# Kernel optimization log

Measured on AMD Instinct MI355X. Metric: run time of the kernel, lower is better.

## Reference

```python
import jax, jax.numpy as jnp
import numpy as np
from jax import lax

SIGMA1, SIGMA2, TRUNCATE = 4.2, 96.0, 4.0


def _gauss_kernel1d(sigma, truncate):
    # scipy-style: radius = int(truncate*sigma + 0.5), normalized Gaussian
    r = int(truncate * sigma + 0.5)
    t = jnp.arange(-r, r + 1, dtype=jnp.float32)
    k = jnp.exp(-0.5 * (t / sigma) ** 2)
    return k / jnp.sum(k)


def _depthwise_conv1d_centered(x_bcl, k):
    # x_bcl: [B, C, L]; k: [K] with K odd. Centered 'same' conv with reflect padding.
    B, C, L = x_bcl.shape
    K = k.shape[0]
    r = (K - 1) // 2
    xp = jnp.pad(x_bcl, ((0, 0), (0, 0), (r, r)), mode='reflect')
    w = jnp.broadcast_to(k[None, None, :], (C, 1, K)).astype(x_bcl.dtype)
    return lax.conv_general_dilated(
        xp, w, window_strides=(1,), padding='VALID',
        feature_group_count=C,
        dimension_numbers=('NCH', 'OIH', 'NCH'))


def setup_inputs() -> dict:
    key = jax.random.key(0)
    x = jax.random.normal(key, (32, 4096, 321), dtype=jnp.float32)  # [B, L, C]
    return {"x": x}


def reference(x) -> jnp.ndarray:
    k1 = _gauss_kernel1d(SIGMA1, TRUNCATE).astype(x.dtype)
    k2 = _gauss_kernel1d(SIGMA2, TRUNCATE).astype(x.dtype)
    x_bcl = jnp.transpose(x, (0, 2, 1))          # [B, C, L]
    y1 = _depthwise_conv1d_centered(x_bcl, k1)   # narrow Gaussian LP
    y2 = _depthwise_conv1d_centered(x_bcl, k2)   # wide Gaussian LP
    seasonal = y1 - y2
    return jnp.transpose(seasonal, (0, 2, 1))    # back to [B, L, C]
```

## Files before the change

### kernel.cpp

```cpp
#include <hip/hip_runtime.h>
#include <math.h>


#define Bdim 32
#define Ldim 4096
#define Cdim 321

#define R1 17
#define K1n 35
#define R2 384
#define K2n 769

#define GA_R 48
#define GA_N 97
#define GB_R 24
#define GB_N 49

#define NG 257
#define NJD 305
#define NGRP_A 20
#define NTJ 33

#define TL 64
#define TROWS 98
#define NLT 64
#define NCT 6
#define NSEG 128

#define GA_OFF 0
#define GB_OFF 128
#define W1_OFF 192
#define K2_OFF 256
#define K2P_OFF 1088
#define E2_OFF 4096
#define D_OFF 4096
#define E_OFF (D_OFF + Bdim*NJD*Cdim)
#define WS_TOT (E_OFF + Bdim*NG*Cdim)

typedef float f32x2 __attribute__((ext_vector_type(2)));

__device__ __forceinline__ int mirror_idx(int a) {
    a = a < 0 ? -a : a;
    a = a > (Ldim - 1) ? 2 * (Ldim - 1) - a : a;
    return a;
}

__device__ __forceinline__ int xcd_swizzle(int bid, int nwg) {
    int q = nwg >> 3, r = nwg & 7;
    int xcd = bid & 7, i = bid >> 3;
    int base = (xcd < r) ? xcd * (q + 1) : r * (q + 1) + (xcd - r) * q;
    return base + i;
}

__device__ __forceinline__ float block_sum_1024(float v, float* partial) {
#pragma unroll
    for (int off = 32; off >= 1; off >>= 1) v += __shfl_down(v, off, 64);
    __syncthreads();
    if ((threadIdx.x & 63) == 0) partial[threadIdx.x >> 6] = v;
    __syncthreads();
    float s = partial[0];
#pragma unroll
    for (int i = 1; i < 16; ++i) s += partial[i];
    return s;
}

__global__ void init_weights_kernel(float* __restrict__ w) {
    __shared__ float partial[16];
    const int tid = threadIdx.x;

    {
        float v = 0.f;
        if (tid < GA_N) { float t = (float)(tid - GA_R) * (1.0f / 12.0f); v = expf(-0.5f * t * t); }
        float s = block_sum_1024(v, partial);
        if (tid < GA_N) w[GA_OFF + tid] = v / s;
    }
    {
        const float sb = sqrtf(96.f * 96.f - 12.f * 12.f) * (1.0f / 16.0f);
        float v = 0.f;
        if (tid < GB_N) { float t = (float)(tid - GB_R) / sb; v = expf(-0.5f * t * t); }
        float s = block_sum_1024(v, partial);
        if (tid < GB_N) w[GB_OFF + tid] = v / s;
    }
    {
        float v = 0.f;
        if (tid < K1n) { float t = (float)(tid - R1) * (1.0f / 4.2f); v = expf(-0.5f * t * t); }
        float s = block_sum_1024(v, partial);
        if (tid < K1n) w[W1_OFF + tid] = v / s;
    }
    {
        float v = 0.f;
        if (tid < K2n) { float t = (float)(tid - R2) * (1.0f / 96.0f); v = expf(-0.5f * t * t); }
        float s = block_sum_1024(v, partial);
        if (tid < K2n) w[K2_OFF + tid] = v / s;
        if (tid < 784) w[K2P_OFF + tid] = (tid < K2n) ? v / s : 0.f;
    }
}

__global__ __launch_bounds__(256) void decimA_kernel(
        const float* __restrict__ x, const float* __restrict__ ga,
        float* __restrict__ d) {
    __shared__ float gs[GA_N];
    if (threadIdx.x < GA_N) gs[threadIdx.x] = ga[threadIdx.x];
    __syncthreads();

    const int lb = xcd_swizzle(blockIdx.x, gridDim.x);
    const int lin = lb * 256 + threadIdx.x;
    const int c = lin % Cdim;
    const int rest = lin / Cdim;
    const int g = rest % NGRP_A;
    const int b = rest / NGRP_A;
    if (b >= Bdim) return;

    const int jj0 = -24 + 16 * g;
    const float* xb = x + b * (Ldim * Cdim) + c;

    float acc[16];
#pragma unroll
    for (int ii = 0; ii < 16; ++ii) acc[ii] = 0.f;

    const bool interior = (jj0 >= 3) && (jj0 <= 237);

#pragma unroll 1
    for (int p = 0; p < 16; ++p) {
        float row[22];
        if (interior) {
            const float* xp = xb + (16 * (jj0 - 3) + p) * Cdim;
#pragma unroll
            for (int i = 0; i < 22; ++i) row[i] = xp[i * (16 * Cdim)];
        } else {
#pragma unroll
            for (int i = 0; i < 22; ++i)
                row[i] = xb[mirror_idx(16 * (jj0 - 3 + i) + p) * Cdim];
        }
#pragma unroll
        for (int q = 0; q < 6; ++q) {
            const float wq = gs[16 * q + p];
#pragma unroll
            for (int ii = 0; ii < 16; ++ii)
                acc[ii] = fmaf(wq, row[ii + q], acc[ii]);
        }
        if (p == 0) {
            const float w6 = gs[96];
#pragma unroll
            for (int ii = 0; ii < 16; ++ii)
                acc[ii] = fmaf(w6, row[ii + 6], acc[ii]);
        }
    }

    const int j0d = jj0 + 24;
    float* db = d + (b * NJD + j0d) * Cdim + c;
#pragma unroll
    for (int ii = 0; ii < 16; ++ii)
        if (j0d + ii < NJD) db[ii * Cdim] = acc[ii];
}

__global__ __launch_bounds__(256) void coarseB_kernel(
        const float* __restrict__ d, const float* __restrict__ gb,
        float* __restrict__ e) {
    __shared__ float gbs[GB_N];
    if (threadIdx.x < GB_N) gbs[threadIdx.x] = gb[threadIdx.x];
    __syncthreads();

    const int lin = blockIdx.x * 256 + threadIdx.x;
    const int c = lin % Cdim;
    const int rest = lin / Cdim;
    const int tj = rest % NTJ;
    const int b = rest / NTJ;
    if (b >= Bdim) return;

    const int j0 = tj * 8;
    const float* db = d + b * (NJD * Cdim) + c;

    float row[56];
#pragma unroll
    for (int r = 0; r < 56; ++r) {
        int idx = j0 + r;
        idx = idx > (NJD - 1) ? (NJD - 1) : idx;
        row[r] = db[idx * Cdim];
    }

    float acc[8];
#pragma unroll
    for (int jj = 0; jj < 8; ++jj) acc[jj] = 0.f;
#pragma unroll
    for (int s = 0; s < GB_N; ++s) {
        const float wv = gbs[s];
#pragma unroll
        for (int jj = 0; jj < 8; ++jj)
            acc[jj] = fmaf(wv, row[s + jj], acc[jj]);
    }

    float* eb = e + (b * NG + j0) * Cdim + c;
#pragma unroll
    for (int jj = 0; jj < 8; ++jj)
        if (j0 + jj < NG) eb[jj * Cdim] = acc[jj];
}

__global__ __launch_bounds__(256, 3) void narrow_lds_kernel(
        const float* __restrict__ x, const float* __restrict__ w1,
        const float* __restrict__ e, float* __restrict__ out) {
    __shared__ float ws[K1n];
    __shared__ float tile[TROWS * 64];
    if (threadIdx.x < K1n) ws[threadIdx.x] = w1[threadIdx.x];

    const int bid = xcd_swizzle(blockIdx.x, gridDim.x);
    const int lt = bid % NLT;
    const int rest = bid / NLT;
    const int ct = rest % NCT;
    const int b = rest / NCT;

    const int c = threadIdx.x & 63;
    const int wv = threadIdx.x >> 6;
    const int c0 = (ct < 5) ? ct * 64 : Cdim - 64;
    const int l0 = lt * TL;
    const float* xb = x + b * (Ldim * Cdim);

    if (lt > 0 && lt < NLT - 1) {
        const float* xp = xb + (l0 - R1) * Cdim + c0 + c;
#pragma unroll
        for (int k = 0; k < 25; ++k) {
            const int r = wv + 4 * k;
            if (r < TROWS) tile[r * 64 + c] = xp[r * Cdim];
        }
    } else {
#pragma unroll
        for (int k = 0; k < 25; ++k) {
            const int r = wv + 4 * k;
            if (r < TROWS) tile[r * 64 + c] = xb[mirror_idx(l0 - R1 + r) * Cdim + c0 + c];
        }
    }
    __syncthreads();

    const int cp = threadIdx.x & 31;
    const int g = threadIdx.x >> 5;
    const int lg = g * 8;

    f32x2 r2[42];
#pragma unroll
    for (int i = 0; i < 42; ++i)
        r2[i] = *reinterpret_cast<const f32x2*>(&tile[(lg + i) * 64 + 2 * cp]);

    f32x2 acc[8];
#pragma unroll
    for (int m = 0; m < 8; ++m) acc[m] = (f32x2)(0.f);
#pragma unroll
    for (int t = 0; t < K1n; ++t) {
        const float wt = ws[t];
        const f32x2 w2 = {wt, wt};
#pragma unroll
        for (int m = 0; m < 8; ++m)
            acc[m] = __builtin_elementwise_fma(w2, r2[t + m], acc[m]);
    }

    const int j = (l0 + lg) >> 4;
    const float f0 = (float)((l0 + lg) & 15);
    const float* eb = e + (b * NG + j) * Cdim + c0 + 2 * cp;
    f32x2 z0 = {eb[0], eb[1]};
    f32x2 z1 = {eb[Cdim], eb[Cdim + 1]};
    f32x2 dz = (z1 - z0) * 0.0625f;

    float* ob = out + (b * Ldim + l0 + lg) * Cdim + c0 + 2 * cp;
#pragma unroll
    for (int m = 0; m < 8; ++m) {
        f32x2 itp = __builtin_elementwise_fma(dz, (f32x2)(f0 + (float)m), z0);
        f32x2 r = acc[m] - itp;
        ob[m * Cdim] = r.x;
        ob[m * Cdim + 1] = r.y;
    }
}

__global__ __launch_bounds__(256, 2) void narrow_reg_kernel(
        const float* __restrict__ x, const float* __restrict__ w1,
        const float* __restrict__ e, float* __restrict__ out) {
    __shared__ float ws[K1n];
    if (threadIdx.x < K1n) ws[threadIdx.x] = w1[threadIdx.x];
    __syncthreads();

    const int lb = xcd_swizzle(blockIdx.x, gridDim.x);
    const int lin = lb * 256 + threadIdx.x;
    const int c = lin % Cdim;
    const int rest = lin / Cdim;
    const int seg = rest % NSEG;
    const int b = rest / NSEG;
    if (b >= Bdim) return;

    const int l0 = seg * 32;
    const float* xb = x + b * (Ldim * Cdim) + c;

    const int j0 = seg * 2;
    const float* eb = e + (b * NG + j0) * Cdim + c;
    const float z0 = eb[0];
    const float z1 = eb[Cdim];
    const float z2 = eb[2 * Cdim];

    float row[66];
    if (seg >= 1 && seg <= 126) {
        const float* xp = xb + (l0 - R1) * Cdim;
#pragma unroll
        for (int i = 0; i < 66; ++i) row[i] = xp[i * Cdim];
    } else {
#pragma unroll
        for (int i = 0; i < 66; ++i)
            row[i] = xb[mirror_idx(l0 - R1 + i) * Cdim];
    }

    float acc[32];
#pragma unroll
    for (int m = 0; m < 32; ++m) acc[m] = 0.f;
#pragma unroll
    for (int t = 0; t < K1n; ++t) {
        const float wt = ws[t];
#pragma unroll
        for (int m = 0; m < 32; ++m)
            acc[m] = fmaf(wt, row[t + m], acc[m]);
    }

    const float d0 = (z1 - z0) * (1.0f / 16.0f);
    const float d1 = (z2 - z1) * (1.0f / 16.0f);
    float* ob = out + (b * Ldim + l0) * Cdim + c;
#pragma unroll
    for (int m = 0; m < 16; ++m)
        ob[m * Cdim] = acc[m] - fmaf(d0, (float)m, z0);
#pragma unroll
    for (int m = 16; m < 32; ++m)
        ob[m * Cdim] = acc[m] - fmaf(d1, (float)(m - 16), z1);
}

#define JPT 16
#define NJG 17
__global__ __launch_bounds__(256, 2) void wide_mid_kernel(
        const float* __restrict__ x, const float* __restrict__ w2p,
        float* __restrict__ z) {
    __shared__ float w2s[784];
    for (int i = threadIdx.x; i < 784; i += 256) w2s[i] = w2p[i];
    __syncthreads();

    const int gid = blockIdx.x * 256 + threadIdx.x;
    const int c = gid % Cdim;
    const int rest = gid / Cdim;
    const int jg = rest % NJG;
    const int b = rest / NJG;
    if (b >= Bdim) return;

    const int j0 = jg * JPT;
    const float* xb = x + b * (Ldim * Cdim) + c;

    float acc[JPT];
#pragma unroll
    for (int jj = 0; jj < JPT; ++jj) acc[jj] = 0.f;

    const bool interior = (j0 >= 24) && (16 * (j0 + 39) + 15 <= Ldim - 1);

#pragma unroll 1
    for (int p = 0; p < 16; ++p) {
        float row[64];
        if (interior) {
            const float* xp = xb + (16 * (j0 - 24) + p) * Cdim;
#pragma unroll
            for (int i = 0; i < 64; ++i) row[i] = xp[i * (16 * Cdim)];
        } else {
#pragma unroll
            for (int i = 0; i < 64; ++i)
                row[i] = xb[mirror_idx(16 * (j0 - 24 + i) + p) * Cdim];
        }
#pragma unroll
        for (int q = 0; q < 49; ++q) {
            const float wq = w2s[q * 16 + p];
#pragma unroll
            for (int jj = 0; jj < JPT; ++jj)
                acc[jj] = fmaf(wq, row[q + jj], acc[jj]);
        }
    }

    float* zb = z + (b * NG + j0) * Cdim + c;
#pragma unroll
    for (int jj = 0; jj < JPT; ++jj)
        if (j0 + jj < NG) zb[jj * Cdim] = acc[jj];
}

__global__ __launch_bounds__(256) void naive_kernel(
        const float* __restrict__ x, const float* __restrict__ w,
        float* __restrict__ out) {
    const int gid = blockIdx.x * 256 + threadIdx.x;
    if (gid >= Bdim * Ldim * Cdim) return;
    const int c = gid % Cdim;
    const int rest = gid / Cdim;
    const int l = rest % Ldim;
    const int b = rest / Ldim;
    const float* xb = x + b * (Ldim * Cdim) + c;
    float a2 = 0.f, a1 = 0.f;
    for (int t = 0; t < K2n; ++t)
        a2 = fmaf(w[K2_OFF + t], xb[mirror_idx(l + t - R2) * Cdim], a2);
#pragma unroll
    for (int t = 0; t < K1n; ++t)
        a1 = fmaf(w[W1_OFF + t], xb[mirror_idx(l + t - R1) * Cdim], a1);
    out[gid] = a1 - a2;
}

extern "C" void kernel_launch(void* const* d_in, const int* in_sizes, int n_in,
                              void* d_out, int out_size, void* d_ws, size_t ws_size,
                              hipStream_t stream) {
    (void)in_sizes; (void)n_in; (void)out_size;
    const float* x = (const float*)d_in[0];
    float* out = (float*)d_out;
    float* w = (float*)d_ws;

    hipLaunchKernelGGL(init_weights_kernel, dim3(1), dim3(1024), 0, stream, w);

    const size_t need_pyr = (size_t)WS_TOT * sizeof(float);
    const size_t need_mid = (size_t)(E2_OFF + Bdim * NG * Cdim) * sizeof(float);

    if (ws_size >= need_pyr) {
        const int a_total = Bdim * NGRP_A * Cdim;
        hipLaunchKernelGGL(decimA_kernel, dim3((a_total + 255) / 256), dim3(256),
                           0, stream, x, w + GA_OFF, w + D_OFF);
        const int b_total = Bdim * NTJ * Cdim;
        hipLaunchKernelGGL(coarseB_kernel, dim3((b_total + 255) / 256), dim3(256),
                           0, stream, w + D_OFF, w + GB_OFF, w + E_OFF);
        const int nblk = Bdim * NCT * NLT;
        hipLaunchKernelGGL(narrow_lds_kernel, dim3(nblk), dim3(256),
                           0, stream, x, w + W1_OFF, w + E_OFF, out);
    } else if (ws_size >= need_mid) {
        const int wide_total = Bdim * NJG * Cdim;
        hipLaunchKernelGGL(wide_mid_kernel, dim3((wide_total + 255) / 256), dim3(256),
                           0, stream, x, w + K2P_OFF, w + E2_OFF);
        const int nar_total = Bdim * NSEG * Cdim;
        hipLaunchKernelGGL(narrow_reg_kernel, dim3((nar_total + 255) / 256), dim3(256),
                           0, stream, x, w + W1_OFF, w + E2_OFF, out);
    } else {
        const int total = Bdim * Ldim * Cdim;
        hipLaunchKernelGGL(naive_kernel, dim3((total + 255) / 256), dim3(256),
                           0, stream, x, w, out);
    }
}
```

Baseline: 167.3 us.

## Double-buffer narrow conv tiles with async global-to-LDS loads, 4 tiles per block

The narrow-filter kernel now processes four consecutive L-tiles per block and stages the next tile into a second LDS buffer with global_load_lds while the current one is computed. The overlapping sixth channel tile is dropped: five 64-channel tiles are used and the last channel (320) is handled by a dedicated wave through an extra LDS column. The LDS row stride is padded to 66. The intent is to hide global load latency and stop recomputing the overlapping channel tile. The cost is fewer blocks (2560 vs 12288), an extra serial pass for the leftover channel, and per-iteration barriers.

```diff
diff --git a/kernel.cpp b/kernel.cpp
--- a/kernel.cpp
+++ b/kernel.cpp
@@ -21,10 +21,13 @@
 #define NGRP_A 20
 #define NTJ 33
 
-#define TL 64
-#define TROWS 98
+#define TLP 64
+#define TRW 98
+#define LSTRIDE 66
 #define NLT 64
-#define NCT 6
+#define NT_PER_BLK 4
+#define NGRP_L 16
+#define NCT5 5
 #define NSEG 128
 
 #define GA_OFF 0
@@ -196,76 +199,110 @@
         if (j0 + jj < NG) eb[jj * Cdim] = acc[jj];
 }
 
-__global__ __launch_bounds__(256, 3) void narrow_lds_kernel(
+__global__ __launch_bounds__(256) void narrow_pipe_kernel(
         const float* __restrict__ x, const float* __restrict__ w1,
         const float* __restrict__ e, float* __restrict__ out) {
     __shared__ float ws[K1n];
-    __shared__ float tile[TROWS * 64];
+    __shared__ float tile[2][TRW * LSTRIDE];
     if (threadIdx.x < K1n) ws[threadIdx.x] = w1[threadIdx.x];
 
     const int bid = xcd_swizzle(blockIdx.x, gridDim.x);
-    const int lt = bid % NLT;
-    const int rest = bid / NLT;
-    const int ct = rest % NCT;
-    const int b = rest / NCT;
-
-    const int c = threadIdx.x & 63;
+    const int g0 = bid & (NGRP_L - 1);
+    const int rest = bid >> 4;
+    const int ct = rest % NCT5;
+    const int b = rest / NCT5;
+
+    const int lane = threadIdx.x & 63;
     const int wv = threadIdx.x >> 6;
-    const int c0 = (ct < 5) ? ct * 64 : Cdim - 64;
-    const int l0 = lt * TL;
+    const int c0 = ct * 64;
     const float* xb = x + b * (Ldim * Cdim);
-
-    if (lt > 0 && lt < NLT - 1) {
-        const float* xp = xb + (l0 - R1) * Cdim + c0 + c;
+    const bool lastct = (ct == NCT5 - 1);
+
+    auto STAGE = [&](int buf, int lt) {
+        const int lbase = lt * TLP - R1;
+        float* tb = &tile[buf][0];
 #pragma unroll
         for (int k = 0; k < 25; ++k) {
             const int r = wv + 4 * k;
-            if (r < TROWS) tile[r * 64 + c] = xp[r * Cdim];
-        }
-    } else {
-#pragma unroll
-        for (int k = 0; k < 25; ++k) {
-            const int r = wv + 4 * k;
-            if (r < TROWS) tile[r * 64 + c] = xb[mirror_idx(l0 - R1 + r) * Cdim + c0 + c];
-        }
-    }
+            if (r < TRW) {
+                const int lrow = mirror_idx(lbase + r);
+                const float* g = xb + lrow * Cdim + c0 + lane;
+                __builtin_amdgcn_global_load_lds(
+                    (const __attribute__((address_space(1))) void*)g,
+                    (__attribute__((address_space(3))) void*)(tb + r * LSTRIDE),
+                    4, 0, 0);
+            }
+        }
+        if (lastct && threadIdx.x < TRW) {
+            const int lrow = mirror_idx(lbase + (int)threadIdx.x);
+            tb[threadIdx.x * LSTRIDE + 64] = xb[lrow * Cdim + 320];
+        }
+    };
+
+    const int lt0 = g0 * NT_PER_BLK;
+    STAGE(0, lt0);
     __syncthreads();
 
     const int cp = threadIdx.x & 31;
     const int g = threadIdx.x >> 5;
     const int lg = g * 8;
 
-    f32x2 r2[42];
-#pragma unroll
-    for (int i = 0; i < 42; ++i)
-        r2[i] = *reinterpret_cast<const f32x2*>(&tile[(lg + i) * 64 + 2 * cp]);
-
-    f32x2 acc[8];
-#pragma unroll
-    for (int m = 0; m < 8; ++m) acc[m] = (f32x2)(0.f);
-#pragma unroll
-    for (int t = 0; t < K1n; ++t) {
-        const float wt = ws[t];
-        const f32x2 w2 = {wt, wt};
-#pragma unroll
-        for (int m = 0; m < 8; ++m)
-            acc[m] = __builtin_elementwise_fma(w2, r2[t + m], acc[m]);
-    }
-
-    const int j = (l0 + lg) >> 4;
-    const float f0 = (float)((l0 + lg) & 15);
-    const float* eb = e + (b * NG + j) * Cdim + c0 + 2 * cp;
-    f32x2 z0 = {eb[0], eb[1]};
-    f32x2 z1 = {eb[Cdim], eb[Cdim + 1]};
-    f32x2 dz = (z1 - z0) * 0.0625f;
-
-    float* ob = out + (b * Ldim + l0 + lg) * Cdim + c0 + 2 * cp;
-#pragma unroll
-    for (int m = 0; m < 8; ++m) {
-        f32x2 itp = __builtin_elementwise_fma(dz, (f32x2)(f0 + (float)m), z0);
-        f32x2 r = acc[m] - itp;
-        ob[m * Cdim] = r.x;
-        ob[m * Cdim + 1] = r.y;
+#pragma unroll 1
+    for (int it = 0; it < NT_PER_BLK; ++it) {
+        const int lt = lt0 + it;
+        const int cur = it & 1;
+        if (it + 1 < NT_PER_BLK) STAGE(cur ^ 1, lt + 1);
+
+        const int l0 = lt * TLP;
+        const float* tb = &tile[cur][0];
+
+        f32x2 r2[42];
+#pragma unroll
+        for (int i = 0; i < 42; ++i)
+            r2[i] = *reinterpret_cast<const f32x2*>(&tb[(lg + i) * LSTRIDE + 2 * cp]);
+
+        f32x2 acc[8];
+#pragma unroll
+        for (int m = 0; m < 8; ++m) acc[m] = (f32x2)(0.f);
+#pragma unroll
+        for (int t = 0; t < K1n; ++t) {
+            const float wt = ws[t];
+            const f32x2 w2 = {wt, wt};
+#pragma unroll
+            for (int m = 0; m < 8; ++m)
+                acc[m] = __builtin_elementwise_fma(w2, r2[t + m], acc[m]);
+        }
+
+        const int j = (l0 + lg) >> 4;
+        const float f0 = (float)((l0 + lg) & 15);
+        const float* eb = e + (b * NG + j) * Cdim + c0 + 2 * cp;
+        f32x2 z0 = {eb[0], eb[1]};
+        f32x2 z1 = {eb[Cdim], eb[Cdim + 1]};
+        f32x2 dz = (z1 - z0) * 0.0625f;
+
+        float* ob = out + (b * Ldim + l0 + lg) * Cdim + c0 + 2 * cp;
+#pragma unroll
+        for (int m = 0; m < 8; ++m) {
+            f32x2 itp = __builtin_elementwise_fma(dz, (f32x2)(f0 + (float)m), z0);
+            f32x2 r = acc[m] - itp;
+            ob[m * Cdim] = r.x;
+            ob[m * Cdim + 1] = r.y;
+        }
+
+        if (lastct && wv == 3) {
+            const int l = l0 + lane;
+            float a = 0.f;
+#pragma unroll
+            for (int t = 0; t < K1n; ++t)
+                a = fmaf(ws[t], tb[(lane + t) * LSTRIDE + 64], a);
+            const int j2 = l >> 4;
+            const float z0s = e[(b * NG + j2) * Cdim + 320];
+            const float z1s = e[(b * NG + j2 + 1) * Cdim + 320];
+            const float itp = fmaf((z1s - z0s) * 0.0625f, (float)(l & 15), z0s);
+            out[(b * Ldim + l) * Cdim + 320] = a - itp;
+        }
+
+        __syncthreads();
     }
 }
 
@@ -417,8 +454,8 @@
         const int b_total = Bdim * NTJ * Cdim;
         hipLaunchKernelGGL(coarseB_kernel, dim3((b_total + 255) / 256), dim3(256),
                            0, stream, w + D_OFF, w + GB_OFF, w + E_OFF);
-        const int nblk = Bdim * NCT * NLT;
-        hipLaunchKernelGGL(narrow_lds_kernel, dim3(nblk), dim3(256),
+        const int nblk = Bdim * NCT5 * NGRP_L;
+        hipLaunchKernelGGL(narrow_pipe_kernel, dim3(nblk), dim3(256),
                            0, stream, x, w + W1_OFF, w + E_OFF, out);
     } else if (ws_size >= need_mid) {
         const int wide_total = Bdim * NJG * Cdim;
```

After: 171.8 us. 2.7% more time.
